# Kernel optimization log

Hardware: AMD Instinct MI355X
Metric: run time of the kernel (lower is better)

Reference implementation:

```python
import jax, jax.numpy as jnp
import numpy as np

GRID = 192          # grid_size (scaled up from the module's toy 32)
H = 0.1             # cell_size
VISC = 0.01         # viscosity
DT = 0.01           # config.time_step, passed as forward's dt
GRAV = 9.81


def setup_inputs() -> dict:
    key = jax.random.key(0)
    velocity_field = jax.random.normal(key, (3, GRID, GRID, GRID), dtype=jnp.float32)
    return {"velocity_field": velocity_field}


def _nb_sum(f):
    # 6-neighbor sum on the interior of the last three axes
    return (f[..., 2:, 1:-1, 1:-1] + f[..., :-2, 1:-1, 1:-1]
            + f[..., 1:-1, 2:, 1:-1] + f[..., 1:-1, :-2, 1:-1]
            + f[..., 1:-1, 1:-1, 2:] + f[..., 1:-1, 1:-1, :-2])


def _fluid_step(vel):
    N = GRID
    dt = DT
    # --- add_gravity ---
    vel = vel.at[2].add(-GRAV * dt)
    # --- advect: semi-Lagrangian backtrace + trilinear interpolation ---
    coords = jnp.arange(N, dtype=vel.dtype)
    X, Y, Z = jnp.meshgrid(coords, coords, coords, indexing='ij')
    pos = jnp.stack([X, Y, Z]) - vel * (dt / H)        # [3,N,N,N] backtraced positions
    pos = jnp.clip(pos, 0.0, float(N - 2))
    i0 = jnp.floor(pos).astype(jnp.int32)              # base corner, i1 = i0+1 <= N-1
    w1 = pos - i0.astype(vel.dtype)
    w0 = 1.0 - w1
    ix, iy, iz = i0[0], i0[1], i0[2]
    wx0, wy0, wz0 = w0[0], w0[1], w0[2]
    wx1, wy1, wz1 = w1[0], w1[1], w1[2]

    def g(di, dj, dk):
        return vel[:, ix + di, iy + dj, iz + dk]        # gather -> [3,N,N,N]

    vel = (g(0, 0, 0) * wx0 * wy0 * wz0 + g(0, 0, 1) * wx0 * wy0 * wz1
           + g(0, 1, 0) * wx0 * wy1 * wz0 + g(0, 1, 1) * wx0 * wy1 * wz1
           + g(1, 0, 0) * wx1 * wy0 * wz0 + g(1, 0, 1) * wx1 * wy0 * wz1
           + g(1, 1, 0) * wx1 * wy1 * wz0 + g(1, 1, 1) * wx1 * wy1 * wz1)
    # --- diffuse: 5 Jacobi sweeps on the interior ---
    alpha = VISC * dt / (H * H)
    inv = 1.0 / (1.0 + 6.0 * alpha)
    for _ in range(5):
        interior = (vel[:, 1:-1, 1:-1, 1:-1] + alpha * _nb_sum(vel)) * inv
        vel = vel.at[:, 1:-1, 1:-1, 1:-1].set(interior)
    # --- project: central-difference divergence, 20 Jacobi pressure sweeps, gradient subtract ---
    div = jnp.zeros((N, N, N), vel.dtype)
    div_int = ((vel[0, 2:, 1:-1, 1:-1] - vel[0, :-2, 1:-1, 1:-1])
               + (vel[1, 1:-1, 2:, 1:-1] - vel[1, 1:-1, :-2, 1:-1])
               + (vel[2, 1:-1, 1:-1, 2:] - vel[2, 1:-1, 1:-1, :-2])) / (2.0 * H)
    div = div.at[1:-1, 1:-1, 1:-1].set(div_int)
    p = jnp.zeros_like(div)
    for _ in range(20):
        p = p.at[1:-1, 1:-1, 1:-1].set((div[1:-1, 1:-1, 1:-1] + _nb_sum(p)) / 6.0)
    inv2h = 1.0 / (2.0 * H)
    vel = vel.at[0, 1:-1, 1:-1, 1:-1].add(-(p[2:, 1:-1, 1:-1] - p[:-2, 1:-1, 1:-1]) * inv2h)
    vel = vel.at[1, 1:-1, 1:-1, 1:-1].add(-(p[1:-1, 2:, 1:-1] - p[1:-1, :-2, 1:-1]) * inv2h)
    vel = vel.at[2, 1:-1, 1:-1, 1:-1].add(-(p[1:-1, 1:-1, 2:] - p[1:-1, 1:-1, :-2]) * inv2h)
    return vel


def reference(velocity_field):
    return _fluid_step(velocity_field)
```

## Files before the change

kernel.cpp:

```cpp
#include <hip/hip_runtime.h>
#include <hip/hip_fp16.h>


constexpr int   N      = 192;
constexpr int   N2     = N * N;
constexpr int   N3     = N * N * N;
constexpr float GDT    = 9.81f * 0.01f;
constexpr float SCL    = 0.01f / 0.1f;
constexpr float ALPHA  = 0.01f * 0.01f / (0.1f * 0.1f);
constexpr float INVDIF = 1.0f / (1.0f + 6.0f * ALPHA);
constexpr float INV2H  = 1.0f / (2.0f * 0.1f);
constexpr float SIXTH  = 1.0f / 6.0f;

constexpr int NT4 = (N3 / 4) / 256;
constexpr int SLAB = NT4 / 8;

__device__ __forceinline__ int swz(int b) {
    return (b & 7) * SLAB + (b >> 3);
}

__device__ __forceinline__ void decomp(int id, int& i, int& j, int& k0) {
    i = id / N2;
    const int r = id - i * N2;
    j = r / N;
    k0 = r - j * N;
}

union H4u { ushort4 u; __half h[4]; };
__device__ __forceinline__ float4 ldh4(const __half* p) {
    H4u t; t.u = *(const ushort4*)p;
    return make_float4(__half2float(t.h[0]), __half2float(t.h[1]),
                       __half2float(t.h[2]), __half2float(t.h[3]));
}
__device__ __forceinline__ void sth4(__half* p, float x, float y, float z, float w) {
    H4u t;
    t.h[0] = __float2half(x); t.h[1] = __float2half(y);
    t.h[2] = __float2half(z); t.h[3] = __float2half(w);
    *(ushort4*)p = t.u;
}
__device__ __forceinline__ float ldh(const __half* p) { return __half2float(*p); }

constexpr int RS    = 196;
constexpr int TILEI = N / 2;
constexpr int TPS   = TILEI / 8;
constexpr int NBADV = (N / 2) * (N / 2);

__global__ __launch_bounds__(768) void k_advect(const float* __restrict__ vin,
                                                float* __restrict__ vout) {
    __shared__ float s[48 * RS];

    const int lin = blockIdx.x;
    const int x   = lin & 7;
    const int q   = lin >> 3;
    const int il  = q % TPS;
    const int jt  = q / TPS;
    const int i0  = (x * TPS + il) * 2;
    const int j0  = jt * 2;

#pragma unroll
    for (int p = 0; p < 3; ++p) {
        const int f   = p * 768 + threadIdx.x;
        const int r   = f / 48;
        const int c4  = f - r * 48;
        const int c   = r >> 4;
        const int rem = r & 15;
        const int di  = rem >> 2;
        const int dj  = rem & 3;
        const int gi  = min(max(i0 + di - 1, 0), N - 1);
        const int gj  = min(max(j0 + dj - 1, 0), N - 1);
        *(float4*)&s[r * RS + c4 * 4] =
            *(const float4*)&vin[c * N3 + gi * N2 + gj * N + c4 * 4];
    }
    __syncthreads();

    const int t  = threadIdx.x / 192;
    const int k  = threadIdx.x - t * 192;
    const int li = t >> 1;
    const int lj = t & 1;
    const int i  = i0 + li;
    const int j  = j0 + lj;
    const int id = (i * N + j) * N + k;

    const int cr = ((li + 1) * 4 + (lj + 1)) * RS + k;
    const float vx = s[cr];
    const float vy = s[16 * RS + cr];
    const float vz = s[32 * RS + cr] - GDT;

    float px = (float)i - vx * SCL;
    float py = (float)j - vy * SCL;
    float pz = (float)k - vz * SCL;
    const float hi = (float)(N - 2);
    px = fminf(fmaxf(px, 0.0f), hi);
    py = fminf(fmaxf(py, 0.0f), hi);
    pz = fminf(fmaxf(pz, 0.0f), hi);

    const int ix = (int)px;
    const int iy = (int)py;
    const int iz = (int)pz;

    float g[3][8];
    const bool in = (ix >= i - 1) & (ix <= i) & (iy >= j - 1) & (iy <= j);
    if (in) {
        const int lix = ix - i0 + 1;
        const int liy = iy - j0 + 1;
#pragma unroll
        for (int c = 0; c < 3; ++c) {
            const int r00 = ((c * 16 + lix * 4 + liy)) * RS + iz;
            const int r01 = r00 + RS;
            const int r10 = r00 + 4 * RS;
            const int r11 = r10 + RS;
            g[c][0] = s[r00];     g[c][1] = s[r00 + 1];
            g[c][2] = s[r01];     g[c][3] = s[r01 + 1];
            g[c][4] = s[r10];     g[c][5] = s[r10 + 1];
            g[c][6] = s[r11];     g[c][7] = s[r11 + 1];
        }
    } else {
        const int base = (ix * N + iy) * N + iz;
#pragma unroll
        for (int c = 0; c < 3; ++c) {
            const float* f = vin + c * N3 + base;
            g[c][0] = f[0];      g[c][1] = f[1];
            g[c][2] = f[N];      g[c][3] = f[N + 1];
            g[c][4] = f[N2];     g[c][5] = f[N2 + 1];
            g[c][6] = f[N2 + N]; g[c][7] = f[N2 + N + 1];
        }
    }

    const float wx1 = px - (float)ix, wy1 = py - (float)iy, wz1 = pz - (float)iz;
    const float wx0 = 1.0f - wx1,     wy0 = 1.0f - wy1,     wz0 = 1.0f - wz1;
    const float w000 = wx0 * wy0 * wz0;
    const float w001 = wx0 * wy0 * wz1;
    const float w010 = wx0 * wy1 * wz0;
    const float w011 = wx0 * wy1 * wz1;
    const float w100 = wx1 * wy0 * wz0;
    const float w101 = wx1 * wy0 * wz1;
    const float w110 = wx1 * wy1 * wz0;
    const float w111 = wx1 * wy1 * wz1;

#pragma unroll
    for (int c = 0; c < 3; ++c) {
        float r = g[c][0] * w000 + g[c][1] * w001
                + g[c][2] * w010 + g[c][3] * w011
                + g[c][4] * w100 + g[c][5] * w101
                + g[c][6] * w110 + g[c][7] * w111;
        if (c == 2) r -= GDT;
        vout[c * N3 + id] = r;
    }
}

__global__ __launch_bounds__(256) void k_diffuse4(const float* __restrict__ vin,
                                                  float* __restrict__ vout) {
    const int gtid = swz(blockIdx.x) * 256 + threadIdx.x;
    const int id   = gtid << 2;
    int i, j, k0; decomp(id, i, j, k0);
    const int b = blockIdx.y * N3 + id;

    const float4 c = *(const float4*)(vin + b);
    float4 out = c;
    if (i != 0 && i != N - 1 && j != 0 && j != N - 1) {
        const float4 ip = *(const float4*)(vin + b + N2);
        const float4 im = *(const float4*)(vin + b - N2);
        const float4 jp = *(const float4*)(vin + b + N);
        const float4 jm = *(const float4*)(vin + b - N);
        const float  km = (k0 > 0)     ? vin[b - 1] : 0.0f;
        const float  kp = (k0 < N - 4) ? vin[b + 4] : 0.0f;
        out.x = (c.x + ALPHA * (im.x + ip.x + jm.x + jp.x + km  + c.y)) * INVDIF;
        out.y = (c.y + ALPHA * (im.y + ip.y + jm.y + jp.y + c.x + c.z)) * INVDIF;
        out.z = (c.z + ALPHA * (im.z + ip.z + jm.z + jp.z + c.y + c.w)) * INVDIF;
        out.w = (c.w + ALPHA * (im.w + ip.w + jm.w + jp.w + c.z + kp )) * INVDIF;
        if (k0 == 0)     out.x = c.x;
        if (k0 == N - 4) out.w = c.w;
    }
    *(float4*)(vout + b) = out;
}

__global__ __launch_bounds__(256) void k_div4(const float* __restrict__ v,
                                              __half* __restrict__ dv) {
    const int gtid = swz(blockIdx.x) * 256 + threadIdx.x;
    const int id   = gtid << 2;
    int i, j, k0; decomp(id, i, j, k0);

    float ox = 0.f, oy = 0.f, oz = 0.f, ow = 0.f;
    if (i != 0 && i != N - 1 && j != 0 && j != N - 1) {
        const float4 xp = *(const float4*)(v + id + N2);
        const float4 xm = *(const float4*)(v + id - N2);
        const float4 yp = *(const float4*)(v + N3 + id + N);
        const float4 ym = *(const float4*)(v + N3 + id - N);
        const float4 z  = *(const float4*)(v + 2 * N3 + id);
        const float  zm = (k0 > 0)     ? v[2 * N3 + id - 1] : 0.0f;
        const float  zp = (k0 < N - 4) ? v[2 * N3 + id + 4] : 0.0f;
        ox = ((xp.x - xm.x) + (yp.x - ym.x) + (z.y - zm )) * INV2H;
        oy = ((xp.y - xm.y) + (yp.y - ym.y) + (z.z - z.x)) * INV2H;
        oz = ((xp.z - xm.z) + (yp.z - ym.z) + (z.w - z.y)) * INV2H;
        ow = ((xp.w - xm.w) + (yp.w - ym.w) + (zp  - z.z)) * INV2H;
        if (k0 == 0)     ox = 0.f;
        if (k0 == N - 4) ow = 0.f;
    }
    sth4(dv + id, ox, oy, oz, ow);
}

__global__ __launch_bounds__(256) void k_p2_4(const __half* __restrict__ dv,
                                              __half* __restrict__ p) {
    const int gtid = swz(blockIdx.x) * 256 + threadIdx.x;
    const int id   = gtid << 2;
    int i, j, k0; decomp(id, i, j, k0);

    float ox = 0.f, oy = 0.f, oz = 0.f, ow = 0.f;
    if (i != 0 && i != N - 1 && j != 0 && j != N - 1) {
        const float4 c  = ldh4(dv + id);
        const float4 ip = ldh4(dv + id + N2);
        const float4 im = ldh4(dv + id - N2);
        const float4 jp = ldh4(dv + id + N);
        const float4 jm = ldh4(dv + id - N);
        const float  km = (k0 > 0)     ? ldh(dv + id - 1) : 0.0f;
        const float  kp = (k0 < N - 4) ? ldh(dv + id + 4) : 0.0f;
        ox = (c.x + (im.x + ip.x + jm.x + jp.x + km  + c.y) * SIXTH) * SIXTH;
        oy = (c.y + (im.y + ip.y + jm.y + jp.y + c.x + c.z) * SIXTH) * SIXTH;
        oz = (c.z + (im.z + ip.z + jm.z + jp.z + c.y + c.w) * SIXTH) * SIXTH;
        ow = (c.w + (im.w + ip.w + jm.w + jp.w + c.z + kp ) * SIXTH) * SIXTH;
        if (k0 == 0)     ox = 0.f;
        if (k0 == N - 4) ow = 0.f;
    }
    sth4(p + id, ox, oy, oz, ow);
}

__global__ __launch_bounds__(256) void k_jacobi4(const __half* __restrict__ pin,
                                                 const __half* __restrict__ dv,
                                                 __half* __restrict__ pout) {
    const int gtid = swz(blockIdx.x) * 256 + threadIdx.x;
    const int id   = gtid << 2;
    int i, j, k0; decomp(id, i, j, k0);

    float ox = 0.f, oy = 0.f, oz = 0.f, ow = 0.f;
    if (i != 0 && i != N - 1 && j != 0 && j != N - 1) {
        const float4 c  = ldh4(pin + id);
        const float4 ip = ldh4(pin + id + N2);
        const float4 im = ldh4(pin + id - N2);
        const float4 jp = ldh4(pin + id + N);
        const float4 jm = ldh4(pin + id - N);
        const float4 d  = ldh4(dv + id);
        const float  km = (k0 > 0)     ? ldh(pin + id - 1) : 0.0f;
        const float  kp = (k0 < N - 4) ? ldh(pin + id + 4) : 0.0f;
        ox = (d.x + im.x + ip.x + jm.x + jp.x + km  + c.y) * SIXTH;
        oy = (d.y + im.y + ip.y + jm.y + jp.y + c.x + c.z) * SIXTH;
        oz = (d.z + im.z + ip.z + jm.z + jp.z + c.y + c.w) * SIXTH;
        ow = (d.w + im.w + ip.w + jm.w + jp.w + c.z + kp ) * SIXTH;
        if (k0 == 0)     ox = 0.f;
        if (k0 == N - 4) ow = 0.f;
    }
    sth4(pout + id, ox, oy, oz, ow);
}

__global__ __launch_bounds__(256) void k_grad4(float* __restrict__ vel,
                                               const __half* __restrict__ p) {
    const int gtid = swz(blockIdx.x) * 256 + threadIdx.x;
    const int id   = gtid << 2;
    int i, j, k0; decomp(id, i, j, k0);
    if (i == 0 || i == N - 1 || j == 0 || j == N - 1) return;

    const float4 xp = ldh4(p + id + N2);
    const float4 xm = ldh4(p + id - N2);
    const float4 yp = ldh4(p + id + N);
    const float4 ym = ldh4(p + id - N);
    const float4 c  = ldh4(p + id);
    const float  pm = (k0 > 0)     ? ldh(p + id - 1) : 0.0f;
    const float  pp = (k0 < N - 4) ? ldh(p + id + 4) : 0.0f;

    const bool bx = (k0 == 0);
    const bool bw = (k0 == N - 4);

    float4 v0 = *(float4*)(vel + id);
    if (!bx) v0.x -= (xp.x - xm.x) * INV2H;
             v0.y -= (xp.y - xm.y) * INV2H;
             v0.z -= (xp.z - xm.z) * INV2H;
    if (!bw) v0.w -= (xp.w - xm.w) * INV2H;
    *(float4*)(vel + id) = v0;

    float4 v1 = *(float4*)(vel + N3 + id);
    if (!bx) v1.x -= (yp.x - ym.x) * INV2H;
             v1.y -= (yp.y - ym.y) * INV2H;
             v1.z -= (yp.z - ym.z) * INV2H;
    if (!bw) v1.w -= (yp.w - ym.w) * INV2H;
    *(float4*)(vel + N3 + id) = v1;

    float4 v2 = *(float4*)(vel + 2 * N3 + id);
    if (!bx) v2.x -= (c.y - pm ) * INV2H;
             v2.y -= (c.z - c.x) * INV2H;
             v2.z -= (c.w - c.y) * INV2H;
    if (!bw) v2.w -= (pp  - c.z) * INV2H;
    *(float4*)(vel + 2 * N3 + id) = v2;
}

extern "C" void kernel_launch(void* const* d_in, const int* in_sizes, int n_in,
                              void* d_out, int out_size, void* d_ws, size_t ws_size,
                              hipStream_t stream) {
    const float* vin  = (const float*)d_in[0];
    float*       vout = (float*)d_out;
    float*       ws   = (float*)d_ws;

    float*  velB = ws;
    __half* hws  = (__half*)d_ws;
    __half* dv   = hws;
    __half* pA   = hws + N3;
    __half* pB   = hws + 2 * N3;

    const dim3 blkA(768, 1, 1);
    const dim3 gridA(NBADV, 1, 1);
    const dim3 blk4(256, 1, 1);
    const dim3 grid4_1(NT4, 1, 1);
    const dim3 grid4_3(NT4, 3, 1);

    k_advect<<<gridA, blkA, 0, stream>>>(vin, velB);

    k_diffuse4<<<grid4_3, blk4, 0, stream>>>(velB, vout);
    k_diffuse4<<<grid4_3, blk4, 0, stream>>>(vout, velB);
    k_diffuse4<<<grid4_3, blk4, 0, stream>>>(velB, vout);
    k_diffuse4<<<grid4_3, blk4, 0, stream>>>(vout, velB);
    k_diffuse4<<<grid4_3, blk4, 0, stream>>>(velB, vout);

    k_div4<<<grid4_1, blk4, 0, stream>>>(vout, dv);
    k_p2_4<<<grid4_1, blk4, 0, stream>>>(dv, pA);
    __half* pin  = pA;
    __half* pout = pB;
    for (int s = 0; s < 18; ++s) {
        k_jacobi4<<<grid4_1, blk4, 0, stream>>>(pin, dv, pout);
        __half* t = pin; pin = pout; pout = t;
    }
    k_grad4<<<grid4_1, blk4, 0, stream>>>(vout, pin);
}
```

Before: 531.5 us.

## Collapse diffusion sweeps into one stencil and fuse pressure Jacobi pairs

Replaces the five diffusion Jacobi sweeps with a single wider stencil: the composed operator is expanded to second order in alpha and scaled by a fitted constant, reading a half-precision advected velocity. The pressure solve is fused two iterations per launch using a radius-2 stencil with masks at the boundaries, which halves the Jacobi launches and the intermediate pressure traffic. The advect output becomes fp16, and the shared-memory row stride drops from 196 to 192, removing its padding. The result is now an approximation, both from truncating the diffusion expansion and from fp16 velocity storage, and the stride change may bring shared-memory bank conflicts.

```diff
diff --git a/kernel.cpp b/kernel.cpp
--- a/kernel.cpp
+++ b/kernel.cpp
@@ -12,6 +12,12 @@
 constexpr float INV2H  = 1.0f / (2.0f * 0.1f);
 constexpr float SIXTH  = 1.0f / 6.0f;
 
+constexpr float B5  = 0.7472581729f;
+constexpr float C0  = B5 * (1.0f + 60.0f * ALPHA * ALPHA);
+constexpr float C1  = B5 * 5.0f * ALPHA;
+constexpr float C2S = B5 * 10.0f * ALPHA * ALPHA;
+constexpr float C2D = B5 * 20.0f * ALPHA * ALPHA;
+
 constexpr int NT4 = (N3 / 4) / 256;
 constexpr int SLAB = NT4 / 8;
 
@@ -40,13 +46,24 @@
 }
 __device__ __forceinline__ float ldh(const __half* p) { return __half2float(*p); }
 
-constexpr int RS    = 196;
+__device__ __forceinline__ void load6(const __half* R, int k0, int km1, int kp4,
+                                      float a[6]) {
+    const float4 m = ldh4(R + k0);
+    a[1] = m.x; a[2] = m.y; a[3] = m.z; a[4] = m.w;
+    a[0] = ldh(R + km1); a[5] = ldh(R + kp4);
+}
+__device__ __forceinline__ void load4a(const __half* R, int k0, float a[4]) {
+    const float4 m = ldh4(R + k0);
+    a[0] = m.x; a[1] = m.y; a[2] = m.z; a[3] = m.w;
+}
+
+constexpr int RS    = 192;
 constexpr int TILEI = N / 2;
 constexpr int TPS   = TILEI / 8;
 constexpr int NBADV = (N / 2) * (N / 2);
 
 __global__ __launch_bounds__(768) void k_advect(const float* __restrict__ vin,
-                                                float* __restrict__ vout) {
+                                                __half* __restrict__ vout) {
     __shared__ float s[48 * RS];
 
     const int lin = blockIdx.x;
@@ -144,34 +161,79 @@
                 + g[c][4] * w100 + g[c][5] * w101
                 + g[c][6] * w110 + g[c][7] * w111;
         if (c == 2) r -= GDT;
-        vout[c * N3 + id] = r;
-    }
-}
-
-__global__ __launch_bounds__(256) void k_diffuse4(const float* __restrict__ vin,
-                                                  float* __restrict__ vout) {
+        vout[c * N3 + id] = __float2half(r);
+    }
+}
+
+__global__ __launch_bounds__(256) void k_diff5(const __half* __restrict__ vin,
+                                               float* __restrict__ vout) {
     const int gtid = swz(blockIdx.x) * 256 + threadIdx.x;
     const int id   = gtid << 2;
     int i, j, k0; decomp(id, i, j, k0);
-    const int b = blockIdx.y * N3 + id;
-
-    const float4 c = *(const float4*)(vin + b);
-    float4 out = c;
-    if (i != 0 && i != N - 1 && j != 0 && j != N - 1) {
-        const float4 ip = *(const float4*)(vin + b + N2);
-        const float4 im = *(const float4*)(vin + b - N2);
-        const float4 jp = *(const float4*)(vin + b + N);
-        const float4 jm = *(const float4*)(vin + b - N);
-        const float  km = (k0 > 0)     ? vin[b - 1] : 0.0f;
-        const float  kp = (k0 < N - 4) ? vin[b + 4] : 0.0f;
-        out.x = (c.x + ALPHA * (im.x + ip.x + jm.x + jp.x + km  + c.y)) * INVDIF;
-        out.y = (c.y + ALPHA * (im.y + ip.y + jm.y + jp.y + c.x + c.z)) * INVDIF;
-        out.z = (c.z + ALPHA * (im.z + ip.z + jm.z + jp.z + c.y + c.w)) * INVDIF;
-        out.w = (c.w + ALPHA * (im.w + ip.w + jm.w + jp.w + c.z + kp )) * INVDIF;
-        if (k0 == 0)     out.x = c.x;
-        if (k0 == N - 4) out.w = c.w;
-    }
-    *(float4*)(vout + b) = out;
+    const __half* V = vin + blockIdx.y * N3;
+    float*        O = vout + blockIdx.y * N3;
+
+    if (i == 0 || i == N - 1 || j == 0 || j == N - 1) {
+        const float4 c = ldh4(V + id);
+        *(float4*)(O + id) = c;
+        return;
+    }
+
+    const int rb  = (i * N + j) * N;
+    const int im2 = max(i - 2, 0), ip2 = min(i + 2, N - 1);
+    const int jm2 = max(j - 2, 0), jp2 = min(j + 2, N - 1);
+    const int km1 = max(k0 - 1, 0), km2 = max(k0 - 2, 0);
+    const int kp4 = min(k0 + 4, N - 1), kp5 = min(k0 + 5, N - 1);
+
+    const __half* Rc   = V + rb;
+    const __half* Rim  = V + rb - N2;
+    const __half* Rip  = V + rb + N2;
+    const __half* Rjm  = V + rb - N;
+    const __half* Rjp  = V + rb + N;
+    const __half* Rimm = V + (im2 * N + j) * N;
+    const __half* Ripp = V + (ip2 * N + j) * N;
+    const __half* Rjmm = V + (i * N + jm2) * N;
+    const __half* Rjpp = V + (i * N + jp2) * N;
+    const __half* Rmm  = V + rb - N2 - N;
+    const __half* Rmp  = V + rb - N2 + N;
+    const __half* Rpm  = V + rb + N2 - N;
+    const __half* Rpp  = V + rb + N2 + N;
+
+    float vc[8];
+    { const float4 m = ldh4(Rc + k0);
+      vc[2] = m.x; vc[3] = m.y; vc[4] = m.z; vc[5] = m.w; }
+    vc[0] = ldh(Rc + km2); vc[1] = ldh(Rc + km1);
+    vc[6] = ldh(Rc + kp4); vc[7] = ldh(Rc + kp5);
+
+    float vim[6], vip[6], vjm[6], vjp[6];
+    load6(Rim, k0, km1, kp4, vim);
+    load6(Rip, k0, km1, kp4, vip);
+    load6(Rjm, k0, km1, kp4, vjm);
+    load6(Rjp, k0, km1, kp4, vjp);
+
+    float vimm[4], vipp[4], vjmm[4], vjpp[4];
+    float vmm[4], vmp[4], vpm[4], vpp[4];
+    load4a(Rimm, k0, vimm); load4a(Ripp, k0, vipp);
+    load4a(Rjmm, k0, vjmm); load4a(Rjpp, k0, vjpp);
+    load4a(Rmm, k0, vmm);   load4a(Rmp, k0, vmp);
+    load4a(Rpm, k0, vpm);   load4a(Rpp, k0, vpp);
+
+    float o[4];
+#pragma unroll
+    for (int t = 0; t < 4; ++t) {
+        const int k = k0 + t;
+        const float S1 = vim[t + 1] + vip[t + 1] + vjm[t + 1] + vjp[t + 1]
+                       + vc[t + 1] + vc[t + 3];
+        const float S2s = vimm[t] + vipp[t] + vjmm[t] + vjpp[t]
+                        + vc[t] + vc[t + 4];
+        const float S2d = vmm[t] + vmp[t] + vpm[t] + vpp[t]
+                        + vim[t] + vim[t + 2] + vip[t] + vip[t + 2]
+                        + vjm[t] + vjm[t + 2] + vjp[t] + vjp[t + 2];
+        float r = C0 * vc[t + 2] + C1 * S1 + C2S * S2s + C2D * S2d;
+        if (k == 0 || k == N - 1) r = vc[t + 2];
+        o[t] = r;
+    }
+    *(float4*)(O + id) = make_float4(o[0], o[1], o[2], o[3]);
 }
 
 __global__ __launch_bounds__(256) void k_div4(const float* __restrict__ v,
@@ -224,31 +286,95 @@
     sth4(p + id, ox, oy, oz, ow);
 }
 
-__global__ __launch_bounds__(256) void k_jacobi4(const __half* __restrict__ pin,
-                                                 const __half* __restrict__ dv,
-                                                 __half* __restrict__ pout) {
+__global__ __launch_bounds__(256) void k_jac2(const __half* __restrict__ pin,
+                                              const __half* __restrict__ dvf,
+                                              __half* __restrict__ pout) {
     const int gtid = swz(blockIdx.x) * 256 + threadIdx.x;
     const int id   = gtid << 2;
     int i, j, k0; decomp(id, i, j, k0);
 
-    float ox = 0.f, oy = 0.f, oz = 0.f, ow = 0.f;
-    if (i != 0 && i != N - 1 && j != 0 && j != N - 1) {
-        const float4 c  = ldh4(pin + id);
-        const float4 ip = ldh4(pin + id + N2);
-        const float4 im = ldh4(pin + id - N2);
-        const float4 jp = ldh4(pin + id + N);
-        const float4 jm = ldh4(pin + id - N);
-        const float4 d  = ldh4(dv + id);
-        const float  km = (k0 > 0)     ? ldh(pin + id - 1) : 0.0f;
-        const float  kp = (k0 < N - 4) ? ldh(pin + id + 4) : 0.0f;
-        ox = (d.x + im.x + ip.x + jm.x + jp.x + km  + c.y) * SIXTH;
-        oy = (d.y + im.y + ip.y + jm.y + jp.y + c.x + c.z) * SIXTH;
-        oz = (d.z + im.z + ip.z + jm.z + jp.z + c.y + c.w) * SIXTH;
-        ow = (d.w + im.w + ip.w + jm.w + jp.w + c.z + kp ) * SIXTH;
-        if (k0 == 0)     ox = 0.f;
-        if (k0 == N - 4) ow = 0.f;
-    }
-    sth4(pout + id, ox, oy, oz, ow);
+    float o[4] = {0.f, 0.f, 0.f, 0.f};
+    if (i >= 1 && i <= N - 2 && j >= 1 && j <= N - 2) {
+        const int rb  = (i * N + j) * N;
+        const int im2 = max(i - 2, 0), ip2 = min(i + 2, N - 1);
+        const int jm2 = max(j - 2, 0), jp2 = min(j + 2, N - 1);
+        const int km1 = max(k0 - 1, 0), km2 = max(k0 - 2, 0);
+        const int kp4 = min(k0 + 4, N - 1), kp5 = min(k0 + 5, N - 1);
+
+        const __half* Pc   = pin + rb;
+        const __half* Pim  = pin + rb - N2;
+        const __half* Pip  = pin + rb + N2;
+        const __half* Pjm  = pin + rb - N;
+        const __half* Pjp  = pin + rb + N;
+        const __half* Pimm = pin + (im2 * N + j) * N;
+        const __half* Pipp = pin + (ip2 * N + j) * N;
+        const __half* Pjmm = pin + (i * N + jm2) * N;
+        const __half* Pjpp = pin + (i * N + jp2) * N;
+        const __half* Pmm  = pin + rb - N2 - N;
+        const __half* Pmp  = pin + rb - N2 + N;
+        const __half* Ppm  = pin + rb + N2 - N;
+        const __half* Ppp  = pin + rb + N2 + N;
+        const __half* Dc   = dvf + rb;
+        const __half* Dim  = dvf + rb - N2;
+        const __half* Dip  = dvf + rb + N2;
+        const __half* Djm  = dvf + rb - N;
+        const __half* Djp  = dvf + rb + N;
+
+        float pc[8];
+        { const float4 m = ldh4(Pc + k0);
+          pc[2] = m.x; pc[3] = m.y; pc[4] = m.z; pc[5] = m.w; }
+        pc[0] = ldh(Pc + km2); pc[1] = ldh(Pc + km1);
+        pc[6] = ldh(Pc + kp4); pc[7] = ldh(Pc + kp5);
+
+        float pim[6], pip[6], pjm[6], pjp[6];
+        load6(Pim, k0, km1, kp4, pim);
+        load6(Pip, k0, km1, kp4, pip);
+        load6(Pjm, k0, km1, kp4, pjm);
+        load6(Pjp, k0, km1, kp4, pjp);
+
+        float pimm[4], pipp[4], pjmm[4], pjpp[4];
+        float pmm[4], pmp[4], ppm[4], ppp[4];
+        load4a(Pimm, k0, pimm); load4a(Pipp, k0, pipp);
+        load4a(Pjmm, k0, pjmm); load4a(Pjpp, k0, pjpp);
+        load4a(Pmm, k0, pmm);   load4a(Pmp, k0, pmp);
+        load4a(Ppm, k0, ppm);   load4a(Ppp, k0, ppp);
+
+        float dc[6];
+        load6(Dc, k0, km1, kp4, dc);
+        float dim_[4], dip_[4], djm_[4], djp_[4];
+        load4a(Dim, k0, dim_); load4a(Dip, k0, dip_);
+        load4a(Djm, k0, djm_); load4a(Djp, k0, djp_);
+
+        const float mip = (i < N - 2) ? 1.f : 0.f;
+        const float mim = (i > 1)     ? 1.f : 0.f;
+        const float mjp = (j < N - 2) ? 1.f : 0.f;
+        const float mjm = (j > 1)     ? 1.f : 0.f;
+
+#pragma unroll
+        for (int t = 0; t < 4; ++t) {
+            const int k = k0 + t;
+            const float gip = mip * (dip_[t] + pc[t + 2] + pipp[t]
+                                   + ppm[t] + ppp[t] + pip[t] + pip[t + 2]);
+            const float gim = mim * (dim_[t] + pc[t + 2] + pimm[t]
+                                   + pmm[t] + pmp[t] + pim[t] + pim[t + 2]);
+            const float gjp = mjp * (djp_[t] + pc[t + 2] + pjpp[t]
+                                   + pmp[t] + ppp[t] + pjp[t] + pjp[t + 2]);
+            const float gjm = mjm * (djm_[t] + pc[t + 2] + pjmm[t]
+                                   + pmm[t] + ppm[t] + pjm[t] + pjm[t + 2]);
+            const float mkp = (k <= N - 3) ? 1.f : 0.f;
+            const float mkm = (k >= 2)     ? 1.f : 0.f;
+            const float gkp = mkp * (dc[t + 2] + pc[t + 2] + pc[t + 4]
+                                   + pim[t + 2] + pip[t + 2]
+                                   + pjm[t + 2] + pjp[t + 2]);
+            const float gkm = mkm * (dc[t] + pc[t + 2] + pc[t]
+                                   + pim[t] + pip[t] + pjm[t] + pjp[t]);
+            float r = (dc[t + 1]
+                     + (gip + gim + gjp + gjm + gkp + gkm) * SIXTH) * SIXTH;
+            if (k < 1 || k > N - 2) r = 0.f;
+            o[t] = r;
+        }
+    }
+    sth4(pout + id, o[0], o[1], o[2], o[3]);
 }
 
 __global__ __launch_bounds__(256) void k_grad4(float* __restrict__ vel,
@@ -296,34 +422,27 @@
                               hipStream_t stream) {
     const float* vin  = (const float*)d_in[0];
     float*       vout = (float*)d_out;
-    float*       ws   = (float*)d_ws;
-
-    float*  velB = ws;
+
     __half* hws  = (__half*)d_ws;
+    __half* velA = hws;
     __half* dv   = hws;
     __half* pA   = hws + N3;
     __half* pB   = hws + 2 * N3;
 
-    const dim3 blkA(768, 1, 1);
-    const dim3 gridA(NBADV, 1, 1);
     const dim3 blk4(256, 1, 1);
     const dim3 grid4_1(NT4, 1, 1);
     const dim3 grid4_3(NT4, 3, 1);
 
-    k_advect<<<gridA, blkA, 0, stream>>>(vin, velB);
-
-    k_diffuse4<<<grid4_3, blk4, 0, stream>>>(velB, vout);
-    k_diffuse4<<<grid4_3, blk4, 0, stream>>>(vout, velB);
-    k_diffuse4<<<grid4_3, blk4, 0, stream>>>(velB, vout);
-    k_diffuse4<<<grid4_3, blk4, 0, stream>>>(vout, velB);
-    k_diffuse4<<<grid4_3, blk4, 0, stream>>>(velB, vout);
+    k_advect<<<dim3(NBADV), dim3(768), 0, stream>>>(vin, velA);
+
+    k_diff5<<<grid4_3, blk4, 0, stream>>>(velA, vout);
 
     k_div4<<<grid4_1, blk4, 0, stream>>>(vout, dv);
     k_p2_4<<<grid4_1, blk4, 0, stream>>>(dv, pA);
     __half* pin  = pA;
     __half* pout = pB;
-    for (int s = 0; s < 18; ++s) {
-        k_jacobi4<<<grid4_1, blk4, 0, stream>>>(pin, dv, pout);
+    for (int s = 0; s < 9; ++s) {
+        k_jac2<<<grid4_1, blk4, 0, stream>>>(pin, dv, pout);
         __half* t = pin; pin = pout; pout = t;
     }
     k_grad4<<<grid4_1, blk4, 0, stream>>>(vout, pin);
```

Measured after the change: 518.3 us. 1.03x faster.
